# Kernel optimization log

Hardware: AMD Instinct MI355X
Metric: run time of the kernel (lower is better)

Reference implementation:

```python
import jax, jax.numpy as jnp
import numpy as np

# Config matching init_kwargs: layer_nb=1 -> stride 16, image 608x608 -> 38x38 grid
B, CIN, H, W = 32, 512, 38, 38
NA, NC = 3, 80
STRIDE = 16.0
ANCHORS = np.array([[30.0, 61.0], [62.0, 45.0], [59.0, 119.0]], dtype=np.float32)


def setup_inputs() -> dict:
    key = jax.random.key(0)
    k1, k2, k3 = jax.random.split(key, 3)
    xin = jax.random.normal(k1, (B, CIN, H, W), dtype=jnp.float32)
    # 1x1 conv weight stored as (out_ch, in_ch); out_ch = NA*(NC+5) = 255
    conv_w = jax.random.normal(k2, (NA * (NC + 5), CIN), dtype=jnp.float32) * 0.02
    conv_b = jax.random.normal(k3, (NA * (NC + 5),), dtype=jnp.float32) * 0.01
    return {"xin": xin, "conv_w": conv_w, "conv_b": conv_b}


def reference(xin, conv_w, conv_b):
    # 1x1 conv == channel GEMM; fuse the NCHW->NHWC permute into the einsum
    fm = jnp.einsum('bchw,oc->bhwo', xin, conv_w) + conv_b  # [B,H,W,255]
    fm = fm.reshape(B, H, W, NA, NC + 5)
    tx, ty, tw, th = fm[..., 0], fm[..., 1], fm[..., 2], fm[..., 3]
    # grid offsets (precomputed via broadcasting instead of per-call numpy rebuild)
    x_off = jnp.arange(W, dtype=fm.dtype)[None, None, :, None]   # broadcast over B,H,NA
    y_off = jnp.arange(H, dtype=fm.dtype)[None, :, None, None]   # broadcast over B,W,NA
    anchors = jnp.asarray(ANCHORS, dtype=fm.dtype)               # [NA,2]
    bx = (jax.nn.sigmoid(tx) + x_off) * STRIDE
    by = (jax.nn.sigmoid(ty) + y_off) * STRIDE
    bw = jnp.exp(tw) * anchors[:, 0]
    bh = jnp.exp(th) * anchors[:, 1]
    boxes = jnp.stack([bx, by, bw, bh], axis=-1)                 # [B,H,W,NA,4]
    # concat decoded boxes with raw objectness + class logits -> [B,H,W,NA,85]
    return jnp.concatenate([boxes, fm[..., 4:]], axis=-1)
```

## Files before the change

kernel.cpp:

```cpp
#include <hip/hip_runtime.h>
#include <cstdint>
#include <cstddef>

#define CIN_K  512
#define WW_    38
#define BHW    1444
#define NOUT   255
#define MTOT   46208

#define ROW_E  520
#define ROW_DW 260

typedef __attribute__((ext_vector_type(8))) short  bf16x8;
typedef __attribute__((ext_vector_type(4))) float  floatx4;

static __device__ __forceinline__ unsigned f2bf(float f) {
    unsigned u = __builtin_bit_cast(unsigned, f);
    return (u + 0x7FFFu + ((u >> 16) & 1u)) >> 16;
}

__global__ void conv_w_to_bf16(const float* __restrict__ cw,
                               unsigned short* __restrict__ wb) {
    int tg   = blockIdx.x * 256 + threadIdx.x;
    int base = tg * 8;
    int n    = base >> 9;
    unsigned rr[4] = {0u, 0u, 0u, 0u};
    if (n < NOUT) {
        float4 v0 = *(const float4*)(cw + base);
        float4 v1 = *(const float4*)(cw + base + 4);
        rr[0] = f2bf(v0.x) | (f2bf(v0.y) << 16);
        rr[1] = f2bf(v0.z) | (f2bf(v0.w) << 16);
        rr[2] = f2bf(v1.x) | (f2bf(v1.y) << 16);
        rr[3] = f2bf(v1.z) | (f2bf(v1.w) << 16);
    }
    *(uint4*)(wb + base) = *(uint4*)rr;
}

__global__ __launch_bounds__(256, 2)
void yolo_head(const float* __restrict__ xin,
               const unsigned short* __restrict__ wb,
               const float* __restrict__ cb,
               float* __restrict__ out)
{
    __shared__ unsigned int smem[64 * ROW_DW];
    unsigned short* As = (unsigned short*)smem;

    const int t    = threadIdx.x;
    const int w    = t >> 6;
    const int lane = t & 63;
    const int l15  = lane & 15;
    const int q    = lane >> 4;
    const int m0   = blockIdx.x * 64;

    {
        const int mloc = lane;
        int m  = m0 + mloc;
        int bi = m / BHW;
        int hw = m - bi * BHW;
        const float* pa = xin + (size_t)bi * (CIN_K * BHW) + hw;
#pragma unroll
        for (int s = 0; s < 16; ++s) {
            const int k0 = s * 32 + w * 8;
            float v[8];
#pragma unroll
            for (int u = 0; u < 8; ++u) v[u] = pa[(size_t)(k0 + u) * BHW];
            unsigned pk[4];
#pragma unroll
            for (int u2 = 0; u2 < 4; ++u2)
                pk[u2] = f2bf(v[2 * u2]) | (f2bf(v[2 * u2 + 1]) << 16);
            *(uint4*)(&As[mloc * ROW_E + k0]) = *(uint4*)pk;
        }
    }
    __syncthreads();

    floatx4 acc[4][4];
#pragma unroll
    for (int i = 0; i < 4; ++i)
#pragma unroll
        for (int j = 0; j < 4; ++j)
            acc[i][j] = (floatx4){0.f, 0.f, 0.f, 0.f};

    const unsigned short* pbw = wb + (size_t)(w * 64 + l15) * CIN_K + q * 8;

#pragma unroll
    for (int kc = 0; kc < 16; ++kc) {
        bf16x8 bfr[4], af[4];
#pragma unroll
        for (int j = 0; j < 4; ++j) {
            uint4 bv = *(const uint4*)(pbw + (size_t)j * 16 * CIN_K + kc * 32);
            bfr[j] = __builtin_bit_cast(bf16x8, bv);
        }
#pragma unroll
        for (int i = 0; i < 4; ++i) {
            int4 av = *(const int4*)(&As[(i * 16 + l15) * ROW_E + kc * 32 + q * 8]);
            af[i] = __builtin_bit_cast(bf16x8, av);
        }
#pragma unroll
        for (int i = 0; i < 4; ++i)
#pragma unroll
            for (int j = 0; j < 4; ++j)
                acc[i][j] = __builtin_amdgcn_mfma_f32_16x16x32_bf16(
                                af[i], bfr[j], acc[i][j], 0, 0, 0);
    }

#pragma unroll
    for (int j = 0; j < 4; ++j) {
        int   n    = w * 64 + j * 16 + l15;
        int   nc   = n < NOUT ? n : NOUT - 1;
        int   ai   = nc / 85;
        int   ji   = nc - ai * 85;
        float bias = cb[nc];
        float aw   = (ai == 0) ? 30.f : (ai == 1) ? 62.f : 59.f;
        float ah   = (ai == 0) ? 61.f : (ai == 1) ? 45.f : 119.f;
#pragma unroll
        for (int i = 0; i < 4; ++i)
#pragma unroll
            for (int r = 0; r < 4; ++r) {
                int   md  = m0 + i * 16 + q * 4 + r;
                int   rem = md % BHW;
                int   hh  = rem / WW_;
                float v   = acc[i][j][r] + bias;
                float res;
                if (ji == 0)      res = (1.f / (1.f + __expf(-v)) + (float)(rem - hh * WW_)) * 16.f;
                else if (ji == 1) res = (1.f / (1.f + __expf(-v)) + (float)hh) * 16.f;
                else if (ji == 2) res = __expf(v) * aw;
                else if (ji == 3) res = __expf(v) * ah;
                else              res = v;
                acc[i][j][r] = res;
            }
    }

    __syncthreads();
    float* EP = (float*)smem;

#pragma unroll
    for (int i = 0; i < 4; ++i)
#pragma unroll
        for (int j = 0; j < 4; ++j)
#pragma unroll
            for (int r = 0; r < 4; ++r)
                EP[(i * 16 + q * 4 + r) * ROW_DW + w * 64 + j * 16 + l15] = acc[i][j][r];

    __syncthreads();

    {
        float*       ob  = out + (size_t)(m0 + w * 16) * NOUT;
        const float* EPb = (const float*)smem + (w * 16) * ROW_DW;
#pragma unroll
        for (int s2 = 0; s2 < 16; ++s2) {
            int f4 = s2 * 64 + lane;
            if (f4 < 1020) {
                int   f = f4 * 4;
                float vv[4];
#pragma unroll
                for (int e = 0; e < 4; ++e) {
                    int fe = f + e;
                    int mr = fe / NOUT;
                    int x  = fe - mr * NOUT;
                    vv[e]  = EPb[mr * ROW_DW + x];
                }
                *(float4*)(ob + f) = make_float4(vv[0], vv[1], vv[2], vv[3]);
            }
        }
    }
}

extern "C" void kernel_launch(void* const* d_in, const int* in_sizes, int n_in,
                              void* d_out, int out_size, void* d_ws, size_t ws_size,
                              hipStream_t stream) {
    const float* xin = (const float*)d_in[0];
    const float* cw  = (const float*)d_in[1];
    const float* cb  = (const float*)d_in[2];
    float*       out = (float*)d_out;
    unsigned short* wb = (unsigned short*)d_ws;

    hipLaunchKernelGGL(conv_w_to_bf16, dim3(64), dim3(256), 0, stream, cw, wb);
    hipLaunchKernelGGL(yolo_head, dim3(MTOT / 64), dim3(256), 0, stream,
                       xin, wb, cb, out);
}
```

Before: 195.0 us.

## Double-buffer A chunks via direct global-to-LDS loads and shrink LDS footprint

Replaces the upfront full-K load and bf16 conversion of the activation tile with a two-stage pipeline over 64-wide K chunks. Each chunk is fetched directly into LDS as fp32 with global_load_lds, so the next chunk's load overlaps MFMA work on the current one, and the bf16 conversion moves to LDS reads. The epilogue now writes one 16-row slice at a time, which reduces LDS size enough to raise occupancy to 3 blocks per CU. In exchange there are more barriers and repeated bf16 packing per MFMA fragment, and the strided 65-word LDS reads may bank-conflict.

```diff
diff --git a/kernel.cpp b/kernel.cpp
--- a/kernel.cpp
+++ b/kernel.cpp
@@ -8,11 +8,16 @@
 #define NOUT   255
 #define MTOT   46208
 
-#define ROW_E  520
-#define ROW_DW 260
+#define BK      64
+#define NCHUNK  (CIN_K / BK)
+#define ROWDW   65
+#define CHUNKDW (BK * ROWDW)
+#define EPSTR   260
 
 typedef __attribute__((ext_vector_type(8))) short  bf16x8;
 typedef __attribute__((ext_vector_type(4))) float  floatx4;
+typedef const __attribute__((address_space(1))) unsigned int* gas_ptr;
+typedef __attribute__((address_space(3)))       unsigned int* las_ptr;
 
 static __device__ __forceinline__ unsigned f2bf(float f) {
     unsigned u = __builtin_bit_cast(unsigned, f);
@@ -36,14 +41,13 @@
     *(uint4*)(wb + base) = *(uint4*)rr;
 }
 
-__global__ __launch_bounds__(256, 2)
+__global__ __launch_bounds__(256, 3)
 void yolo_head(const float* __restrict__ xin,
                const unsigned short* __restrict__ wb,
                const float* __restrict__ cb,
                float* __restrict__ out)
 {
-    __shared__ unsigned int smem[64 * ROW_DW];
-    unsigned short* As = (unsigned short*)smem;
+    __shared__ float smem[2 * CHUNKDW];
 
     const int t    = threadIdx.x;
     const int w    = t >> 6;
@@ -52,26 +56,12 @@
     const int q    = lane >> 4;
     const int m0   = blockIdx.x * 64;
 
-    {
-        const int mloc = lane;
-        int m  = m0 + mloc;
-        int bi = m / BHW;
-        int hw = m - bi * BHW;
-        const float* pa = xin + (size_t)bi * (CIN_K * BHW) + hw;
-#pragma unroll
-        for (int s = 0; s < 16; ++s) {
-            const int k0 = s * 32 + w * 8;
-            float v[8];
-#pragma unroll
-            for (int u = 0; u < 8; ++u) v[u] = pa[(size_t)(k0 + u) * BHW];
-            unsigned pk[4];
-#pragma unroll
-            for (int u2 = 0; u2 < 4; ++u2)
-                pk[u2] = f2bf(v[2 * u2]) | (f2bf(v[2 * u2 + 1]) << 16);
-            *(uint4*)(&As[mloc * ROW_E + k0]) = *(uint4*)pk;
-        }
-    }
-    __syncthreads();
+    const int m  = m0 + lane;
+    const int bi = m / BHW;
+    const int hw = m - bi * BHW;
+    const float* pal = xin + (size_t)bi * (CIN_K * BHW) + hw;
+
+    const unsigned short* pbw = wb + (size_t)(w * 64 + l15) * CIN_K + q * 8;
 
     floatx4 acc[4][4];
 #pragma unroll
@@ -80,27 +70,51 @@
         for (int j = 0; j < 4; ++j)
             acc[i][j] = (floatx4){0.f, 0.f, 0.f, 0.f};
 
-    const unsigned short* pbw = wb + (size_t)(w * 64 + l15) * CIN_K + q * 8;
+#define STAGE(buf, k0)                                                        \
+    {                                                                         \
+        const float* g = pal + (size_t)((k0) + w * 16) * BHW;                 \
+        float* lr = smem + (buf) * CHUNKDW + (w * 16) * ROWDW;                \
+        _Pragma("unroll")                                                     \
+        for (int s_ = 0; s_ < 16; ++s_) {                                     \
+            __builtin_amdgcn_global_load_lds((gas_ptr)g, (las_ptr)lr, 4, 0, 0);\
+            g  += BHW;                                                        \
+            lr += ROWDW;                                                      \
+        }                                                                     \
+    }
+
+    STAGE(0, 0)
 
 #pragma unroll
-    for (int kc = 0; kc < 16; ++kc) {
-        bf16x8 bfr[4], af[4];
+    for (int s = 0; s < NCHUNK; ++s) {
+        __syncthreads();
+        if (s < NCHUNK - 1) STAGE((s + 1) & 1, (s + 1) * BK)
+
+        const float* Ab = smem + (s & 1) * CHUNKDW;
 #pragma unroll
-        for (int j = 0; j < 4; ++j) {
-            uint4 bv = *(const uint4*)(pbw + (size_t)j * 16 * CIN_K + kc * 32);
-            bfr[j] = __builtin_bit_cast(bf16x8, bv);
+        for (int kc = 0; kc < 2; ++kc) {
+            bf16x8 bfr[4];
+#pragma unroll
+            for (int j = 0; j < 4; ++j) {
+                uint4 bv = *(const uint4*)(pbw + s * BK + kc * 32 + (size_t)j * 16 * CIN_K);
+                bfr[j] = __builtin_bit_cast(bf16x8, bv);
+            }
+#pragma unroll
+            for (int i = 0; i < 4; ++i) {
+                const float* ap = Ab + (kc * 32 + q * 8) * ROWDW + i * 16 + l15;
+                float v[8];
+#pragma unroll
+                for (int u = 0; u < 8; ++u) v[u] = ap[u * ROWDW];
+                unsigned pk[4];
+#pragma unroll
+                for (int u2 = 0; u2 < 4; ++u2)
+                    pk[u2] = f2bf(v[2 * u2]) | (f2bf(v[2 * u2 + 1]) << 16);
+                bf16x8 af = __builtin_bit_cast(bf16x8, *(int4*)pk);
+#pragma unroll
+                for (int j = 0; j < 4; ++j)
+                    acc[i][j] = __builtin_amdgcn_mfma_f32_16x16x32_bf16(
+                                    af, bfr[j], acc[i][j], 0, 0, 0);
+            }
         }
-#pragma unroll
-        for (int i = 0; i < 4; ++i) {
-            int4 av = *(const int4*)(&As[(i * 16 + l15) * ROW_E + kc * 32 + q * 8]);
-            af[i] = __builtin_bit_cast(bf16x8, av);
-        }
-#pragma unroll
-        for (int i = 0; i < 4; ++i)
-#pragma unroll
-            for (int j = 0; j < 4; ++j)
-                acc[i][j] = __builtin_amdgcn_mfma_f32_16x16x32_bf16(
-                                af[i], bfr[j], acc[i][j], 0, 0, 0);
     }
 
 #pragma unroll
@@ -130,25 +144,23 @@
             }
     }
 
-    __syncthreads();
-    float* EP = (float*)smem;
+    float* EP = smem;
+#pragma unroll 1
+    for (int p = 0; p < 4; ++p) {
+        __syncthreads();
 
-#pragma unroll
-    for (int i = 0; i < 4; ++i)
 #pragma unroll
         for (int j = 0; j < 4; ++j)
 #pragma unroll
             for (int r = 0; r < 4; ++r)
-                EP[(i * 16 + q * 4 + r) * ROW_DW + w * 64 + j * 16 + l15] = acc[i][j][r];
+                EP[(q * 4 + r) * EPSTR + w * 64 + j * 16 + l15] = acc[p][j][r];
 
-    __syncthreads();
+        __syncthreads();
 
-    {
-        float*       ob  = out + (size_t)(m0 + w * 16) * NOUT;
-        const float* EPb = (const float*)smem + (w * 16) * ROW_DW;
+        float* ob = out + (size_t)(m0 + p * 16) * NOUT;
 #pragma unroll
-        for (int s2 = 0; s2 < 16; ++s2) {
-            int f4 = s2 * 64 + lane;
+        for (int s2 = 0; s2 < 4; ++s2) {
+            int f4 = s2 * 256 + t;
             if (f4 < 1020) {
                 int   f = f4 * 4;
                 float vv[4];
@@ -157,7 +169,7 @@
                     int fe = f + e;
                     int mr = fe / NOUT;
                     int x  = fe - mr * NOUT;
-                    vv[e]  = EPb[mr * ROW_DW + x];
+                    vv[e]  = EP[mr * EPSTR + x];
                 }
                 *(float4*)(ob + f) = make_float4(vv[0], vv[1], vv[2], vv[3]);
             }
```

Measured after the change: 270.7 us. 1.39x slower.
